# Optimization experiments

Measured on AMD Instinct MI355X. Metric: run time of the kernel, lower is better.

## Reference

```python
import jax, jax.numpy as jnp
import numpy as np

N, E, T, F, H, OUT, HORIZON = 50000, 1600000, 12, 16, 128, 3, 6
TARGET_IDX = (0, 1, 2)


def setup_inputs() -> dict:
    key = jax.random.key(0)
    ks = jax.random.split(key, 20)
    inp = {
        'x_seq': jax.random.normal(ks[0], (T, N, F), jnp.float32),
        'ei_seq': jax.random.randint(ks[1], (T, 2, E), 0, N, jnp.int32),
        'ea_seq': jax.random.uniform(ks[2], (T, E), jnp.float32),
        'mask_seq': jax.random.bernoulli(ks[3], 0.9, (T, N)),
    }
    sF = 1.0 / np.sqrt(F)
    s2H = 1.0 / np.sqrt(2 * H)
    sH = 1.0 / np.sqrt(H)
    # GCNConv weights (x @ W, W: [F,H]) + biases for z, r, h gates
    for i, g in enumerate(['z', 'r', 'h']):
        inp['Wc' + g] = jax.random.normal(ks[4 + i], (F, H), jnp.float32) * sF
        inp['bc' + g] = jnp.zeros((H,), jnp.float32)
        # Linear(2H, H) stored as [2H, H] for x @ W
        inp['Wl' + g] = jax.random.normal(ks[8 + i], (2 * H, H), jnp.float32) * s2H
        inp['bl' + g] = jnp.zeros((H,), jnp.float32)
    inp['head_W'] = jax.random.normal(ks[12], (H, OUT), jnp.float32) * sH
    inp['head_b'] = jnp.zeros((OUT,), jnp.float32)
    return inp


def _gcn(x, src, dst, ew, W, b):
    # GCNConv with self-loops and symmetric normalization
    loop = jnp.arange(N, dtype=src.dtype)
    s = jnp.concatenate([src, loop])
    d = jnp.concatenate([dst, loop])
    w = jnp.concatenate([ew, jnp.ones((N,), ew.dtype)])
    deg = jax.ops.segment_sum(w, d, num_segments=N)
    dinv = jnp.where(deg > 0, jax.lax.rsqrt(jnp.maximum(deg, 1e-12)), 0.0)
    norm = dinv[s] * w * dinv[d]                      # [E+N]
    xw = x @ W                                        # [N,H]
    return jax.ops.segment_sum(norm[:, None] * xw[s], d, num_segments=N) + b


def _tgcn_cell(x, ei, ew, h, p):
    src, dst = ei[0], ei[1]
    z = jax.nn.sigmoid(
        jnp.concatenate([_gcn(x, src, dst, ew, p['Wcz'], p['bcz']), h], axis=1) @ p['Wlz'] + p['blz'])
    r = jax.nn.sigmoid(
        jnp.concatenate([_gcn(x, src, dst, ew, p['Wcr'], p['bcr']), h], axis=1) @ p['Wlr'] + p['blr'])
    h_tilde = jnp.tanh(
        jnp.concatenate([_gcn(x, src, dst, ew, p['Wch'], p['bch']), h * r], axis=1) @ p['Wlh'] + p['blh'])
    return z * h + (1.0 - z) * h_tilde


def reference(x_seq, ei_seq, ea_seq, mask_seq,
              Wcz, bcz, Wlz, blz, Wcr, bcr, Wlr, blr, Wch, bch, Wlh, blh,
              head_W, head_b):
    p = dict(Wcz=Wcz, bcz=bcz, Wlz=Wlz, blz=blz, Wcr=Wcr, bcr=bcr,
             Wlr=Wlr, blr=blr, Wch=Wch, bch=bch, Wlh=Wlh, blh=blh)

    def step(carry, inputs):
        h_state, seen = carry
        x, ei, ew, m = inputs
        # h_dict lookup: only nodes present now AND seen before carry state
        h_prev = jnp.where((m & seen)[:, None], h_state, 0.0)
        h_new = _tgcn_cell(x, ei, ew, h_prev, p)
        h_state = jnp.where(m[:, None], h_new, h_state)   # h_dict scatter update
        return (h_state, seen | m), None

    init = (jnp.zeros((N, H), x_seq.dtype), jnp.zeros((N,), bool))
    (h_state, _), _ = jax.lax.scan(step, init, (x_seq, ei_seq, ea_seq, mask_seq))

    # final gather: nodes present at last step are all in h_dict after the loop
    h_prev = jnp.where(mask_seq[-1][:, None], h_state, 0.0)
    x_last, ei_last, ew_last = x_seq[-1], ei_seq[-1], ea_seq[-1]
    ti = jnp.array(TARGET_IDX)
    preds = []
    for _ in range(HORIZON):
        inp = x_last if not preds else x_last.at[:, ti].set(preds[-1])
        h_new = _tgcn_cell(inp, ei_last, ew_last, h_prev, p)
        preds.append(h_new @ head_W + head_b)   # dropout is identity in eval
        h_prev = h_new
    return jnp.stack(preds, axis=0)             # [HORIZON, N, OUT]
```

## Files before the change

kernel.cpp:

```cpp
#include <hip/hip_runtime.h>
#include <math.h>

#define NN 50000
#define TT 12
#define EE 1600000
#define FF 16
#define HH 128
#define CHK 4096
#define NCH 391
#define BKT 128
#define NBINS 391
#define CAP 6144
#define RP 50016
#define CGB 782
#define AH_STR 136
#define AX_STR 40
#define HC_STR 136
#define BKROW 160

typedef _Float16 half8_t __attribute__((ext_vector_type(8)));
typedef float floatx4 __attribute__((ext_vector_type(4)));

__device__ __forceinline__ float h16_to_f(unsigned short u) {
    _Float16 h; __builtin_memcpy(&h, &u, 2); return (float)h;
}
__device__ __forceinline__ unsigned short f_to_h16(float f) {
    _Float16 h = (_Float16)f; unsigned short u; __builtin_memcpy(&u, &h, 2); return u;
}
__device__ __forceinline__ float fsig(float x) {
    return 1.0f / (1.0f + exp2f(-1.44269504f * x));
}
__device__ __forceinline__ float ftanh(float x) {
    return 2.0f / (1.0f + exp2f(-2.88539009f * x)) - 1.0f;
}

__global__ void detect_mask(const unsigned char* __restrict__ m, int* __restrict__ flag) {
    __shared__ int cnt[2];
    if (threadIdx.x < 2) cnt[threadIdx.x] = 0;
    __syncthreads();
    int a = 0, b = 0;
    for (int base = 0; base < 4096; base += 256) {
        int idx = base + threadIdx.x;
        unsigned char v = m[idx];
        int r = idx & 3;
        if (v) { if (r == 0) a++; else if (r == 1) b++; }
    }
    atomicAdd(&cnt[0], a);
    atomicAdd(&cnt[1], b);
    __syncthreads();
    if (threadIdx.x == 0) flag[0] = cnt[1] > 0 ? 0 : (cnt[0] > 0 ? 1 : 2);
}

__global__ void build_masks(const void* __restrict__ mask, const int* __restrict__ flag,
                            unsigned char* __restrict__ hm, unsigned char* __restrict__ mc) {
    int n = blockIdx.x * 256 + threadIdx.x;
    if (n >= NN) return;
    int mode = flag[0];
    bool seen = false;
    for (int t = 0; t < TT; t++) {
        int idx = t * NN + n;
        bool m;
        if (mode == 0)      m = ((const unsigned char*)mask)[idx] != 0;
        else if (mode == 1) m = ((const int*)mask)[idx] != 0;
        else                m = ((const float*)mask)[idx] != 0.0f;
        hm[idx] = (m && seen) ? 1 : 0;
        mc[idx] = m ? 1 : 0;
        seen = seen || m;
    }
}

__global__ void hist_kernel(const int* __restrict__ ei, int* __restrict__ chunkHist) {
    __shared__ int h[NBINS + 1];
    int c = blockIdx.x, t = blockIdx.y, tid = threadIdx.x;
    for (int i = tid; i < NBINS; i += 256) h[i] = 0;
    __syncthreads();
    const int* dstp = ei + (size_t)(2 * t + 1) * EE;
    int e0 = c * CHK;
    for (int i = tid; i < CHK; i += 256) {
        int e = e0 + i;
        if (e < EE) atomicAdd(&h[dstp[e] >> 7], 1);
    }
    __syncthreads();
    for (int i = tid; i < NBINS; i += 256)
        chunkHist[((size_t)t * NBINS + i) * NCH + c] = h[i];
}

__global__ void scan_kernel(int* __restrict__ buf) {
    __shared__ int ps[1024];
    const int L = NBINS * NCH;
    const int PER = 150;
    int t = blockIdx.x, tid = threadIdx.x;
    int* a = buf + (size_t)t * L;
    int i0 = tid * PER, i1 = min(i0 + PER, L);
    int s = 0;
    for (int i = i0; i < i1; i++) s += a[i];
    ps[tid] = s;
    __syncthreads();
    for (int off = 1; off < 1024; off <<= 1) {
        int v = (tid >= off) ? ps[tid - off] : 0;
        __syncthreads();
        ps[tid] += v;
        __syncthreads();
    }
    int base = (tid == 0) ? 0 : ps[tid - 1];
    for (int i = i0; i < i1; i++) { int v = a[i]; a[i] = base; base += v; }
}

__launch_bounds__(256)
__global__ void scatter_kernel(const int* __restrict__ ei, const float* __restrict__ ea,
                               const int* __restrict__ chunkOff, uint2* __restrict__ E2,
                               int batch) {
    __shared__ uint2 sorted[CHK];
    __shared__ int cnt[NBINS];
    __shared__ int sA[NBINS], sB[NBINS];
    __shared__ int start[NBINS], gbase[NBINS];
    int c = blockIdx.x, y = blockIdx.y, tid = threadIdx.x;
    int t = batch * 6 + y;
    for (int i = tid; i < NBINS; i += 256) {
        cnt[i] = 0;
        gbase[i] = chunkOff[((size_t)t * NBINS + i) * NCH + c];
    }
    __syncthreads();
    const int* srcp = ei + (size_t)(2 * t) * EE;
    const int* dstp = ei + (size_t)(2 * t + 1) * EE;
    const float* wp = ea + (size_t)t * EE;
    int e0 = c * CHK;
    int m = min(CHK, EE - e0);
    uint2 rec[16];
    int rank[16];
#pragma unroll
    for (int k = 0; k < 16; k++) {
        int i = k * 256 + tid;
        rank[k] = -1;
        if (i < m) {
            int e = e0 + i;
            unsigned int s = (unsigned int)srcp[e];
            unsigned int d = (unsigned int)dstp[e];
            float wv = wp[e];
            rec[k].x = s | (d << 16);
            rec[k].y = __float_as_uint(wv);
            rank[k] = atomicAdd(&cnt[d >> 7], 1);
        }
    }
    __syncthreads();
    for (int i = tid; i < NBINS; i += 256) sA[i] = cnt[i];
    __syncthreads();
    int pp = 0;
    for (int off = 1; off < NBINS; off <<= 1) {
        if (pp == 0) {
            for (int i = tid; i < NBINS; i += 256)
                sB[i] = (i >= off) ? sA[i] + sA[i - off] : sA[i];
        } else {
            for (int i = tid; i < NBINS; i += 256)
                sA[i] = (i >= off) ? sB[i] + sB[i - off] : sB[i];
        }
        pp ^= 1;
        __syncthreads();
    }
    const int* inc = pp ? sB : sA;
    for (int i = tid; i < NBINS; i += 256) start[i] = inc[i] - cnt[i];
    __syncthreads();
#pragma unroll
    for (int k = 0; k < 16; k++) {
        if (rank[k] >= 0) {
            int b = rec[k].x >> 23;
            sorted[start[b] + rank[k]] = rec[k];
        }
    }
    __syncthreads();
    uint2* outp = E2 + (size_t)y * EE;
    for (int i = tid; i < m; i += 256) {
        uint2 r = sorted[i];
        int b = r.x >> 23;
        outp[gbase[b] + (i - start[b])] = r;
    }
}

__launch_bounds__(256)
__global__ void sortbin_kernel(const uint2* __restrict__ E2, const int* __restrict__ chunkHist,
                               unsigned int* __restrict__ E1, int* __restrict__ rowptr,
                               float* __restrict__ dinvG, int batch) {
    __shared__ uint2 es[CAP];
    __shared__ int cnt[BKT];
    __shared__ float wsm[BKT];
    __shared__ int cur[BKT];
    int b = blockIdx.x, y = blockIdx.y, tid = threadIdx.x;
    int t = batch * 6 + y;
    const uint2* gE = E2 + (size_t)y * EE;
    unsigned int* oE = E1 + (size_t)t * EE;
    const int* off = chunkHist + (size_t)t * NBINS * NCH;
    int e0 = off[b * NCH];
    int e1 = (b == NBINS - 1) ? EE : off[(b + 1) * NCH];
    int seg = e1 - e0;
    for (int i = tid; i < seg; i += 256) es[i] = gE[e0 + i];
    if (tid < BKT) { cnt[tid] = 0; wsm[tid] = 0.0f; }
    __syncthreads();
    for (int i = tid; i < seg; i += 256) {
        int dl = (es[i].x >> 16) & 127;
        atomicAdd(&cnt[dl], 1);
        atomicAdd(&wsm[dl], __uint_as_float(es[i].y));
    }
    __syncthreads();
    int ogv = (tid < BKT) ? cnt[tid] : 0;
    for (int o = 1; o < BKT; o <<= 1) {
        int u = (tid < BKT && tid >= o) ? cnt[tid - o] : 0;
        __syncthreads();
        if (tid < BKT) cnt[tid] += u;
        __syncthreads();
    }
    if (tid < BKT) {
        int exc = cnt[tid] - ogv;
        cur[tid] = exc;
        float dv = rsqrtf(1.0f + wsm[tid]);
        wsm[tid] = dv;
        int node = b * BKT + tid;
        if (node <= NN) {
            rowptr[(size_t)t * RP + node] = e0 + exc;
            if (node < NN) dinvG[(size_t)t * NN + node] = dv;
        }
    }
    __syncthreads();
    for (int i = tid; i < seg; i += 256) {
        uint2 p = es[i];
        int dl = (p.x >> 16) & 127;
        int pos = atomicAdd(&cur[dl], 1);
        float wv = __uint_as_float(p.y) * wsm[dl];
        oE[e0 + pos] = (p.x & 0xFFFF) | ((unsigned int)f_to_h16(wv) << 16);
    }
}

__global__ void xs_kernel(const float* __restrict__ x, const float* __restrict__ dinvG,
                          _Float16* __restrict__ xs16) {
    int gid = blockIdx.x * 256 + threadIdx.x;
    int tn = gid >> 2;
    float dd = dinvG[tn];
    float4 v = ((const float4*)x)[gid];
    _Float16 h[4] = {(_Float16)(dd * v.x), (_Float16)(dd * v.y),
                     (_Float16)(dd * v.z), (_Float16)(dd * v.w)};
    uint2 o;
    __builtin_memcpy(&o, h, 8);
    ((uint2*)xs16)[gid] = o;
}

__global__ void gather_csr(const unsigned int* __restrict__ E1, const int* __restrict__ rowptr,
                           const float* __restrict__ dinvG, const _Float16* __restrict__ xs16,
                           _Float16* __restrict__ xagg16) {
    int t = blockIdx.y;
    int n = blockIdx.x * 4 + (threadIdx.x >> 6);
    if (n >= NN) return;
    int lane = threadIdx.x & 63;
    int eo = lane >> 3, fp = lane & 7;
    const unsigned int* gE = E1 + (size_t)t * EE;
    const _Float16* xs = xs16 + (size_t)t * NN * FF;
    int r0 = rowptr[(size_t)t * RP + n], r1 = rowptr[(size_t)t * RP + n + 1];
    float a0 = 0.0f, a1 = 0.0f;
    for (int e = r0 + eo; e < r1; e += 8) {
        unsigned int rec = gE[e];
        float wv = h16_to_f((unsigned short)(rec >> 16));
        unsigned int xp = *(const unsigned int*)(xs + (size_t)(rec & 0xFFFF) * FF + 2 * fp);
        a0 += wv * h16_to_f((unsigned short)(xp & 0xFFFF));
        a1 += wv * h16_to_f((unsigned short)(xp >> 16));
    }
    a0 += __shfl_xor(a0, 8);  a1 += __shfl_xor(a1, 8);
    a0 += __shfl_xor(a0, 16); a1 += __shfl_xor(a1, 16);
    a0 += __shfl_xor(a0, 32); a1 += __shfl_xor(a1, 32);
    if (eo == 0) {
        float dd = dinvG[(size_t)t * NN + n];
        unsigned int xp = *(const unsigned int*)(xs + (size_t)n * FF + 2 * fp);
        float o0 = a0 + dd * h16_to_f((unsigned short)(xp & 0xFFFF));
        float o1 = a1 + dd * h16_to_f((unsigned short)(xp >> 16));
        unsigned int pack = (unsigned int)f_to_h16(o0) | ((unsigned int)f_to_h16(o1) << 16);
        ((unsigned int*)(xagg16 + ((size_t)t * NN + n) * FF))[fp] = pack;
    }
}

__global__ void gather3_csr(const unsigned int* __restrict__ E1, const int* __restrict__ rowptr,
                            const float* __restrict__ dinvG, const float* __restrict__ predsc,
                            _Float16* __restrict__ xaggH16) {
    int n = blockIdx.x * 4 + (threadIdx.x >> 6);
    if (n >= NN) return;
    int lane = threadIdx.x & 63;
    int eo = lane >> 2, f = lane & 3;
    const unsigned int* gE = E1 + (size_t)11 * EE;
    const float* dv = dinvG + (size_t)11 * NN;
    int r0 = rowptr[(size_t)11 * RP + n], r1 = rowptr[(size_t)11 * RP + n + 1];
    float acc = 0.0f;
    for (int e = r0 + eo; e < r1; e += 16) {
        unsigned int rec = gE[e];
        float wv = h16_to_f((unsigned short)(rec >> 16));
        if (f < 3) acc += wv * predsc[(size_t)(rec & 0xFFFF) * 4 + f];
    }
    acc += __shfl_xor(acc, 4);
    acc += __shfl_xor(acc, 8);
    acc += __shfl_xor(acc, 16);
    acc += __shfl_xor(acc, 32);
    if (lane < 3) {
        float res = acc + dv[n] * predsc[(size_t)n * 4 + f];
        xaggH16[(size_t)n * FF + f] = (_Float16)res;
    }
}

__global__ void weight_kernel(const float* Wc0, const float* bc0, const float* Wl0, const float* bl0,
                              const float* Wc1, const float* bc1, const float* Wl1, const float* bl1,
                              const float* Wc2, const float* bc2, const float* Wl2, const float* bl2,
                              _Float16* __restrict__ BcatT, float* __restrict__ beff) {
    __shared__ float WcS[FF][HH];
    int g = blockIdx.x;
    int n = threadIdx.x;
    const float* Wc = g == 0 ? Wc0 : (g == 1 ? Wc1 : Wc2);
    const float* bc = g == 0 ? bc0 : (g == 1 ? bc1 : bc2);
    const float* Wl = g == 0 ? Wl0 : (g == 1 ? Wl1 : Wl2);
    const float* bl = g == 0 ? bl0 : (g == 1 ? bl1 : bl2);
    for (int q = 0; q < FF; q++) WcS[q][n] = Wc[q * HH + n];
    __syncthreads();
    float acc[FF];
#pragma unroll
    for (int i = 0; i < FF; i++) acc[i] = 0.0f;
    float accb = 0.0f;
    for (int k = 0; k < HH; k++) {
        float wl = Wl[k * HH + n];
        accb += bc[k] * wl;
#pragma unroll
        for (int i = 0; i < FF; i++) acc[i] += WcS[i][k] * wl;
    }
    _Float16* row = BcatT + ((size_t)g * HH + n) * BKROW;
    for (int j = 0; j < HH; j++) row[j] = (_Float16)Wl[(size_t)(HH + j) * HH + n];
#pragma unroll
    for (int i = 0; i < FF; i++) row[HH + i] = (_Float16)acc[i];
#pragma unroll
    for (int i = 144; i < 160; i++) row[i] = (_Float16)0.0f;
    beff[g * HH + n] = bl[n] + accb;
}

__launch_bounds__(256, 2)
__global__ void cellseq_kernel(const _Float16* __restrict__ xaggBase,
                               _Float16* __restrict__ hio,
                               const _Float16* __restrict__ BcatT,
                               const float* __restrict__ beff,
                               const unsigned char* __restrict__ hmAll,
                               const unsigned char* __restrict__ mcAll,
                               int nt) {
    __shared__ _Float16 Ah[64 * AH_STR];
    __shared__ _Float16 Ax[64 * AX_STR];
    __shared__ _Float16 Hc[64 * HC_STR];
    const int tid = threadIdx.x;
    const int m0 = blockIdx.x * 64;
    const int lane = tid & 63;
    const int w = tid >> 6;
    const int mrow = lane & 15;
    const int quad = lane >> 4;
    const int c0 = w * 32;
    const bool rec = (hmAll != nullptr);

    half8_t bz[2][5], br[2][5];
#pragma unroll
    for (int c = 0; c < 2; c++) {
        int col = c0 + c * 16 + mrow;
#pragma unroll
        for (int ks = 0; ks < 5; ks++) {
            bz[c][ks] = *(const half8_t*)(BcatT + (size_t)col * BKROW + ks * 32 + quad * 8);
            br[c][ks] = *(const half8_t*)(BcatT + (size_t)(HH + col) * BKROW + ks * 32 + quad * 8);
        }
    }
    float bzv[2], brv[2], bhv[2];
#pragma unroll
    for (int c = 0; c < 2; c++) {
        int col = c0 + c * 16 + mrow;
        bzv[c] = beff[col];
        brv[c] = beff[HH + col];
        bhv[c] = beff[2 * HH + col];
    }

    for (int idx = tid; idx < 128; idx += 256) {
        int row = idx >> 1, q = idx & 1;
        *(uint4*)(Ax + row * AX_STR + 16 + q * 8) = make_uint4(0, 0, 0, 0);
    }
    if (rec) {
        for (int idx = tid; idx < 1024; idx += 256) {
            int row = idx >> 4, q = idx & 15;
            *(uint4*)(Hc + row * HC_STR + q * 8) = make_uint4(0, 0, 0, 0);
        }
    }
    __syncthreads();

    for (int t = 0; t < nt; t++) {
        const _Float16* xa = xaggBase + (size_t)t * NN * FF;
        const unsigned char* hm = rec ? (hmAll + (size_t)t * NN) : nullptr;
        for (int idx = tid; idx < 1024; idx += 256) {
            int row = idx >> 4, q = idx & 15;
            int g = m0 + row;
            uint4 v = make_uint4(0, 0, 0, 0);
            if (rec) {
                if (g < NN && hm[g]) v = *(const uint4*)(Hc + row * HC_STR + q * 8);
            } else {
                if (g < NN) v = *(const uint4*)(hio + (size_t)g * HH + q * 8);
            }
            *(uint4*)(Ah + row * AH_STR + q * 8) = v;
        }
        for (int idx = tid; idx < 128; idx += 256) {
            int row = idx >> 1, q = idx & 1;
            int g = m0 + row;
            uint4 v = make_uint4(0, 0, 0, 0);
            if (g < NN) v = *(const uint4*)(xa + (size_t)g * FF + q * 8);
            *(uint4*)(Ax + row * AX_STR + q * 8) = v;
        }
        __syncthreads();

        floatx4 zacc[4][2], racc[4][2];
#pragma unroll
        for (int m = 0; m < 4; m++)
#pragma unroll
            for (int c = 0; c < 2; c++)
#pragma unroll
                for (int i = 0; i < 4; i++) { zacc[m][c][i] = 0.0f; racc[m][c][i] = 0.0f; }
#pragma unroll
        for (int m = 0; m < 4; m++) {
            half8_t a[5];
#pragma unroll
            for (int ks = 0; ks < 4; ks++)
                a[ks] = *(const half8_t*)(Ah + (m * 16 + mrow) * AH_STR + ks * 32 + quad * 8);
            a[4] = *(const half8_t*)(Ax + (m * 16 + mrow) * AX_STR + quad * 8);
#pragma unroll
            for (int c = 0; c < 2; c++) {
#pragma unroll
                for (int ks = 0; ks < 5; ks++)
                    zacc[m][c] = __builtin_amdgcn_mfma_f32_16x16x32_f16(a[ks], bz[c][ks], zacc[m][c], 0, 0, 0);
#pragma unroll
                for (int ks = 0; ks < 5; ks++)
                    racc[m][c] = __builtin_amdgcn_mfma_f32_16x16x32_f16(a[ks], br[c][ks], racc[m][c], 0, 0, 0);
            }
        }
        _Float16 hprev[32];
#pragma unroll
        for (int m = 0; m < 4; m++)
#pragma unroll
            for (int c = 0; c < 2; c++)
#pragma unroll
                for (int i = 0; i < 4; i++)
                    hprev[(m * 2 + c) * 4 + i] =
                        Ah[(m * 16 + quad * 4 + i) * AH_STR + c0 + c * 16 + mrow];
        __syncthreads();

        half8_t bh[2][5];
#pragma unroll
        for (int c = 0; c < 2; c++) {
            int col = c0 + c * 16 + mrow;
#pragma unroll
            for (int ks = 0; ks < 5; ks++)
                bh[c][ks] = *(const half8_t*)(BcatT + (size_t)(2 * HH + col) * BKROW + ks * 32 + quad * 8);
        }
#pragma unroll
        for (int m = 0; m < 4; m++)
#pragma unroll
            for (int c = 0; c < 2; c++)
#pragma unroll
                for (int i = 0; i < 4; i++) {
                    int row = m * 16 + quad * 4 + i;
                    float rv = fsig(racc[m][c][i] + brv[c]);
                    Ah[row * AH_STR + c0 + c * 16 + mrow] =
                        (_Float16)((float)hprev[(m * 2 + c) * 4 + i] * rv);
                }
        __syncthreads();

        floatx4 hacc[4][2];
#pragma unroll
        for (int m = 0; m < 4; m++)
#pragma unroll
            for (int c = 0; c < 2; c++)
#pragma unroll
                for (int i = 0; i < 4; i++) hacc[m][c][i] = 0.0f;
#pragma unroll
        for (int m = 0; m < 4; m++) {
            half8_t a[5];
#pragma unroll
            for (int ks = 0; ks < 4; ks++)
                a[ks] = *(const half8_t*)(Ah + (m * 16 + mrow) * AH_STR + ks * 32 + quad * 8);
            a[4] = *(const half8_t*)(Ax + (m * 16 + mrow) * AX_STR + quad * 8);
#pragma unroll
            for (int c = 0; c < 2; c++)
#pragma unroll
                for (int ks = 0; ks < 5; ks++)
                    hacc[m][c] = __builtin_amdgcn_mfma_f32_16x16x32_f16(a[ks], bh[c][ks], hacc[m][c], 0, 0, 0);
        }
        const unsigned char* mc = rec ? (mcAll + (size_t)t * NN) : nullptr;
#pragma unroll
        for (int m = 0; m < 4; m++)
#pragma unroll
            for (int c = 0; c < 2; c++)
#pragma unroll
                for (int i = 0; i < 4; i++) {
                    int row = m * 16 + quad * 4 + i;
                    int g = m0 + row;
                    if (g < NN) {
                        int col = c0 + c * 16 + mrow;
                        float z = fsig(zacc[m][c][i] + bzv[c]);
                        float ht = ftanh(hacc[m][c][i] + bhv[c]);
                        float hp = (float)hprev[(m * 2 + c) * 4 + i];
                        float hn = z * hp + (1.0f - z) * ht;
                        if (rec) {
                            if (mc[g]) Hc[row * HC_STR + col] = (_Float16)hn;
                        } else {
                            hio[(size_t)g * HH + col] = (_Float16)hn;
                        }
                    }
                }
        __syncthreads();
    }

    if (rec) {
        const unsigned char* mcL = mcAll + (size_t)(nt - 1) * NN;
        for (int idx = tid; idx < 1024; idx += 256) {
            int row = idx >> 4, q = idx & 15;
            int g = m0 + row;
            if (g < NN) {
                uint4 v = make_uint4(0, 0, 0, 0);
                if (mcL[g]) v = *(const uint4*)(Hc + row * HC_STR + q * 8);
                *(uint4*)(hio + (size_t)g * HH + q * 8) = v;
            }
        }
    }
}

__global__ void head_kernel(const _Float16* __restrict__ hp, const float* __restrict__ headW,
                            const float* __restrict__ headb, const float* __restrict__ dinv11,
                            float* __restrict__ out, float* __restrict__ predsc) {
    int node = (blockIdx.x * 256 + threadIdx.x) >> 6;
    int lane = threadIdx.x & 63;
    if (node >= NN) return;
    const _Float16* h = hp + (size_t)node * HH;
    float h0 = (float)h[lane], h1 = (float)h[64 + lane];
    float s0 = h0 * headW[lane * 3 + 0] + h1 * headW[(64 + lane) * 3 + 0];
    float s1 = h0 * headW[lane * 3 + 1] + h1 * headW[(64 + lane) * 3 + 1];
    float s2 = h0 * headW[lane * 3 + 2] + h1 * headW[(64 + lane) * 3 + 2];
#pragma unroll
    for (int off = 32; off > 0; off >>= 1) {
        s0 += __shfl_down(s0, off);
        s1 += __shfl_down(s1, off);
        s2 += __shfl_down(s2, off);
    }
    if (lane == 0) {
        float o0 = s0 + headb[0], o1 = s1 + headb[1], o2 = s2 + headb[2];
        out[(size_t)node * 3 + 0] = o0;
        out[(size_t)node * 3 + 1] = o1;
        out[(size_t)node * 3 + 2] = o2;
        float dd = dinv11[node];
        predsc[(size_t)node * 4 + 0] = dd * o0;
        predsc[(size_t)node * 4 + 1] = dd * o1;
        predsc[(size_t)node * 4 + 2] = dd * o2;
    }
}

extern "C" void kernel_launch(void* const* d_in, const int* in_sizes, int n_in,
                              void* d_out, int out_size, void* d_ws, size_t ws_size,
                              hipStream_t stream) {
    const float* x = (const float*)d_in[0];
    const int* ei = (const int*)d_in[1];
    const float* ea = (const float*)d_in[2];
    const void* mask = d_in[3];
    const float* Wc[3] = {(const float*)d_in[4], (const float*)d_in[8], (const float*)d_in[12]};
    const float* bc[3] = {(const float*)d_in[5], (const float*)d_in[9], (const float*)d_in[13]};
    const float* Wl[3] = {(const float*)d_in[6], (const float*)d_in[10], (const float*)d_in[14]};
    const float* bl[3] = {(const float*)d_in[7], (const float*)d_in[11], (const float*)d_in[15]};
    const float* headW = (const float*)d_in[16];
    const float* headb = (const float*)d_in[17];
    float* out = (float*)d_out;

    char* w = (char*)d_ws;
    auto alloc = [&](size_t bytes) {
        char* p = w;
        w += (bytes + 255) & ~(size_t)255;
        return p;
    };
    float* dinv = (float*)alloc((size_t)TT * NN * 4);
    _Float16* xagg16 = (_Float16*)alloc((size_t)TT * NN * FF * 2);
    _Float16* xaggH16 = (_Float16*)alloc((size_t)NN * FF * 2);
    _Float16* xs16 = (_Float16*)alloc((size_t)TT * NN * FF * 2);
    int* chunkHist = (int*)alloc((size_t)TT * NBINS * NCH * 4);
    int* rowptr = (int*)alloc((size_t)TT * RP * 4);
    unsigned int* E1 = (unsigned int*)alloc((size_t)TT * EE * 4);
    uint2* E2 = (uint2*)alloc((size_t)6 * EE * 8);
    _Float16* BcatT = (_Float16*)alloc((size_t)3 * HH * BKROW * 2);
    float* beff = (float*)alloc(3 * HH * 4);
    float* predsc = (float*)alloc((size_t)NN * 4 * 4);
    unsigned char* hm = (unsigned char*)alloc((size_t)TT * NN);
    unsigned char* mc = (unsigned char*)alloc((size_t)TT * NN);
    int* flag = (int*)alloc(64);

    _Float16* hph = (_Float16*)E2;

    detect_mask<<<1, 256, 0, stream>>>((const unsigned char*)mask, flag);
    build_masks<<<(NN + 255) / 256, 256, 0, stream>>>(mask, flag, hm, mc);

    hist_kernel<<<dim3(NCH, TT), 256, 0, stream>>>(ei, chunkHist);
    scan_kernel<<<TT, 1024, 0, stream>>>(chunkHist);
    for (int b = 0; b < 2; b++) {
        scatter_kernel<<<dim3(NCH, 6), 256, 0, stream>>>(ei, ea, chunkHist, E2, b);
        sortbin_kernel<<<dim3(NBINS, 6), 256, 0, stream>>>(E2, chunkHist, E1, rowptr, dinv, b);
    }
    xs_kernel<<<TT * NN * 4 / 256, 256, 0, stream>>>(x, dinv, xs16);
    gather_csr<<<dim3((NN + 3) / 4, TT), 256, 0, stream>>>(E1, rowptr, dinv, xs16, xagg16);

    weight_kernel<<<3, 128, 0, stream>>>(Wc[0], bc[0], Wl[0], bl[0],
                                         Wc[1], bc[1], Wl[1], bl[1],
                                         Wc[2], bc[2], Wl[2], bl[2], BcatT, beff);

    cellseq_kernel<<<CGB, 256, 0, stream>>>(xagg16, hph, BcatT, beff, hm, mc, TT);

    hipMemcpyAsync(xaggH16, xagg16 + (size_t)11 * NN * FF, (size_t)NN * FF * 2,
                   hipMemcpyDeviceToDevice, stream);

    for (int k = 0; k < 6; k++) {
        const _Float16* xa = (k == 0) ? (xagg16 + (size_t)11 * NN * FF) : xaggH16;
        cellseq_kernel<<<CGB, 256, 0, stream>>>(xa, hph, BcatT, beff, nullptr, nullptr, 1);
        head_kernel<<<NN * 64 / 256, 256, 0, stream>>>(hph, headW, headb, dinv + (size_t)11 * NN,
                                                       out + (size_t)k * NN * 3, predsc);
        if (k < 5) {
            gather3_csr<<<(NN + 3) / 4, 256, 0, stream>>>(E1, rowptr, dinv, predsc, xaggH16);
        }
    }
}
```

Before: 2.045 ms.

## Restructure GRU cell kernel to 512 threads with transposed MFMA operands

Doubles the cell kernel block to 8 waves, with each wave owning 16 output columns instead of 32. Gate weights are reloaded per step instead of being held in registers. The MFMA operands are swapped so each lane holds 4 contiguous columns, which enables packed 8-byte LDS and global stores. The reset-gated state goes to a separate LDS buffer, which removes one barrier per step. The aim is to cut register pressure and raise occupancy, at the cost of extra weight loads from global memory each step and more LDS per block.

```diff
diff --git a/kernel.cpp b/kernel.cpp
--- a/kernel.cpp
+++ b/kernel.cpp
@@ -332,15 +332,16 @@
     beff[g * HH + n] = bl[n] + accb;
 }
 
-__launch_bounds__(256, 2)
+__launch_bounds__(512, 4)
 __global__ void cellseq_kernel(const _Float16* __restrict__ xaggBase,
                                _Float16* __restrict__ hio,
                                const _Float16* __restrict__ BcatT,
                                const float* __restrict__ beff,
                                const unsigned char* __restrict__ hmAll,
                                const unsigned char* __restrict__ mcAll,
-                               int nt) {
+                               int nsteps) {
     __shared__ _Float16 Ah[64 * AH_STR];
+    __shared__ _Float16 Ar[64 * AH_STR];
     __shared__ _Float16 Ax[64 * AX_STR];
     __shared__ _Float16 Hc[64 * HC_STR];
     const int tid = threadIdx.x;
@@ -349,44 +350,36 @@
     const int w = tid >> 6;
     const int mrow = lane & 15;
     const int quad = lane >> 4;
-    const int c0 = w * 32;
+    const int col0 = w * 16;
+    const int cb = col0 + quad * 4;
     const bool rec = (hmAll != nullptr);
 
-    half8_t bz[2][5], br[2][5];
-#pragma unroll
-    for (int c = 0; c < 2; c++) {
-        int col = c0 + c * 16 + mrow;
-#pragma unroll
-        for (int ks = 0; ks < 5; ks++) {
-            bz[c][ks] = *(const half8_t*)(BcatT + (size_t)col * BKROW + ks * 32 + quad * 8);
-            br[c][ks] = *(const half8_t*)(BcatT + (size_t)(HH + col) * BKROW + ks * 32 + quad * 8);
-        }
-    }
-    float bzv[2], brv[2], bhv[2];
-#pragma unroll
-    for (int c = 0; c < 2; c++) {
-        int col = c0 + c * 16 + mrow;
-        bzv[c] = beff[col];
-        brv[c] = beff[HH + col];
-        bhv[c] = beff[2 * HH + col];
-    }
-
-    for (int idx = tid; idx < 128; idx += 256) {
+    const float4 bz4 = *(const float4*)(beff + cb);
+    const float4 br4 = *(const float4*)(beff + HH + cb);
+    const float4 bh4 = *(const float4*)(beff + 2 * HH + cb);
+
+    const _Float16* Wzp = BcatT + (size_t)(col0 + mrow) * BKROW + quad * 8;
+    const _Float16* Wrp = Wzp + (size_t)HH * BKROW;
+    const _Float16* Whp = Wzp + (size_t)2 * HH * BKROW;
+
+    for (int idx = tid; idx < 128; idx += 512) {
         int row = idx >> 1, q = idx & 1;
         *(uint4*)(Ax + row * AX_STR + 16 + q * 8) = make_uint4(0, 0, 0, 0);
     }
     if (rec) {
-        for (int idx = tid; idx < 1024; idx += 256) {
+        for (int idx = tid; idx < 1024; idx += 512) {
             int row = idx >> 4, q = idx & 15;
             *(uint4*)(Hc + row * HC_STR + q * 8) = make_uint4(0, 0, 0, 0);
         }
     }
     __syncthreads();
 
-    for (int t = 0; t < nt; t++) {
+    for (int t = 0; t < nsteps; t++) {
         const _Float16* xa = xaggBase + (size_t)t * NN * FF;
         const unsigned char* hm = rec ? (hmAll + (size_t)t * NN) : nullptr;
-        for (int idx = tid; idx < 1024; idx += 256) {
+        const unsigned char* mc = rec ? (mcAll + (size_t)t * NN) : nullptr;
+
+        for (int idx = tid; idx < 1024; idx += 512) {
             int row = idx >> 4, q = idx & 15;
             int g = m0 + row;
             uint4 v = make_uint4(0, 0, 0, 0);
@@ -397,7 +390,7 @@
             }
             *(uint4*)(Ah + row * AH_STR + q * 8) = v;
         }
-        for (int idx = tid; idx < 128; idx += 256) {
+        for (int idx = tid; idx < 128; idx += 512) {
             int row = idx >> 1, q = idx & 1;
             int g = m0 + row;
             uint4 v = make_uint4(0, 0, 0, 0);
@@ -406,110 +399,88 @@
         }
         __syncthreads();
 
-        floatx4 zacc[4][2], racc[4][2];
-#pragma unroll
-        for (int m = 0; m < 4; m++)
-#pragma unroll
-            for (int c = 0; c < 2; c++)
-#pragma unroll
-                for (int i = 0; i < 4; i++) { zacc[m][c][i] = 0.0f; racc[m][c][i] = 0.0f; }
-#pragma unroll
-        for (int m = 0; m < 4; m++) {
-            half8_t a[5];
-#pragma unroll
-            for (int ks = 0; ks < 4; ks++)
-                a[ks] = *(const half8_t*)(Ah + (m * 16 + mrow) * AH_STR + ks * 32 + quad * 8);
-            a[4] = *(const half8_t*)(Ax + (m * 16 + mrow) * AX_STR + quad * 8);
-#pragma unroll
-            for (int c = 0; c < 2; c++) {
-#pragma unroll
-                for (int ks = 0; ks < 5; ks++)
-                    zacc[m][c] = __builtin_amdgcn_mfma_f32_16x16x32_f16(a[ks], bz[c][ks], zacc[m][c], 0, 0, 0);
-#pragma unroll
-                for (int ks = 0; ks < 5; ks++)
-                    racc[m][c] = __builtin_amdgcn_mfma_f32_16x16x32_f16(a[ks], br[c][ks], racc[m][c], 0, 0, 0);
+        half8_t wz[5], wr[5];
+#pragma unroll
+        for (int ks = 0; ks < 5; ks++) {
+            wz[ks] = *(const half8_t*)(Wzp + ks * 32);
+            wr[ks] = *(const half8_t*)(Wrp + ks * 32);
+        }
+        floatx4 zacc[4];
+        unsigned int hpw[4][2];
+#pragma unroll
+        for (int nt = 0; nt < 4; nt++) {
+            const _Float16* hxp = Ah + (nt * 16 + mrow) * AH_STR + quad * 8;
+            half8_t hx[5];
+#pragma unroll
+            for (int ks = 0; ks < 4; ks++) hx[ks] = *(const half8_t*)(hxp + ks * 32);
+            hx[4] = *(const half8_t*)(Ax + (nt * 16 + mrow) * AX_STR + quad * 8);
+            floatx4 za = {0.0f, 0.0f, 0.0f, 0.0f}, ra = {0.0f, 0.0f, 0.0f, 0.0f};
+#pragma unroll
+            for (int ks = 0; ks < 5; ks++)
+                za = __builtin_amdgcn_mfma_f32_16x16x32_f16(wz[ks], hx[ks], za, 0, 0, 0);
+#pragma unroll
+            for (int ks = 0; ks < 5; ks++)
+                ra = __builtin_amdgcn_mfma_f32_16x16x32_f16(wr[ks], hx[ks], ra, 0, 0, 0);
+            zacc[nt] = za;
+            uint2 hp = *(const uint2*)(Ah + (nt * 16 + mrow) * AH_STR + cb);
+            hpw[nt][0] = hp.x; hpw[nt][1] = hp.y;
+            float r0 = fsig(ra[0] + br4.x), r1 = fsig(ra[1] + br4.y);
+            float r2 = fsig(ra[2] + br4.z), r3 = fsig(ra[3] + br4.w);
+            float hp0 = h16_to_f((unsigned short)(hp.x & 0xFFFF));
+            float hp1 = h16_to_f((unsigned short)(hp.x >> 16));
+            float hp2 = h16_to_f((unsigned short)(hp.y & 0xFFFF));
+            float hp3 = h16_to_f((unsigned short)(hp.y >> 16));
+            uint2 o;
+            o.x = (unsigned int)f_to_h16(hp0 * r0) | ((unsigned int)f_to_h16(hp1 * r1) << 16);
+            o.y = (unsigned int)f_to_h16(hp2 * r2) | ((unsigned int)f_to_h16(hp3 * r3) << 16);
+            *(uint2*)(Ar + (nt * 16 + mrow) * AH_STR + cb) = o;
+        }
+        __syncthreads();
+
+        half8_t wh[5];
+#pragma unroll
+        for (int ks = 0; ks < 5; ks++) wh[ks] = *(const half8_t*)(Whp + ks * 32);
+#pragma unroll
+        for (int nt = 0; nt < 4; nt++) {
+            const _Float16* hxp = Ar + (nt * 16 + mrow) * AH_STR + quad * 8;
+            half8_t hx[5];
+#pragma unroll
+            for (int ks = 0; ks < 4; ks++) hx[ks] = *(const half8_t*)(hxp + ks * 32);
+            hx[4] = *(const half8_t*)(Ax + (nt * 16 + mrow) * AX_STR + quad * 8);
+            floatx4 ha = {0.0f, 0.0f, 0.0f, 0.0f};
+#pragma unroll
+            for (int ks = 0; ks < 5; ks++)
+                ha = __builtin_amdgcn_mfma_f32_16x16x32_f16(wh[ks], hx[ks], ha, 0, 0, 0);
+            int g = m0 + nt * 16 + mrow;
+            if (g < NN) {
+                float z0 = fsig(zacc[nt][0] + bz4.x), z1 = fsig(zacc[nt][1] + bz4.y);
+                float z2 = fsig(zacc[nt][2] + bz4.z), z3 = fsig(zacc[nt][3] + bz4.w);
+                float t0 = ftanh(ha[0] + bh4.x), t1 = ftanh(ha[1] + bh4.y);
+                float t2 = ftanh(ha[2] + bh4.z), t3 = ftanh(ha[3] + bh4.w);
+                float hp0 = h16_to_f((unsigned short)(hpw[nt][0] & 0xFFFF));
+                float hp1 = h16_to_f((unsigned short)(hpw[nt][0] >> 16));
+                float hp2 = h16_to_f((unsigned short)(hpw[nt][1] & 0xFFFF));
+                float hp3 = h16_to_f((unsigned short)(hpw[nt][1] >> 16));
+                float n0 = z0 * hp0 + (1.0f - z0) * t0;
+                float n1 = z1 * hp1 + (1.0f - z1) * t1;
+                float n2 = z2 * hp2 + (1.0f - z2) * t2;
+                float n3 = z3 * hp3 + (1.0f - z3) * t3;
+                uint2 o;
+                o.x = (unsigned int)f_to_h16(n0) | ((unsigned int)f_to_h16(n1) << 16);
+                o.y = (unsigned int)f_to_h16(n2) | ((unsigned int)f_to_h16(n3) << 16);
+                if (rec) {
+                    if (mc[g]) *(uint2*)(Hc + (nt * 16 + mrow) * HC_STR + cb) = o;
+                } else {
+                    *(uint2*)(hio + (size_t)g * HH + cb) = o;
+                }
             }
         }
-        _Float16 hprev[32];
-#pragma unroll
-        for (int m = 0; m < 4; m++)
-#pragma unroll
-            for (int c = 0; c < 2; c++)
-#pragma unroll
-                for (int i = 0; i < 4; i++)
-                    hprev[(m * 2 + c) * 4 + i] =
-                        Ah[(m * 16 + quad * 4 + i) * AH_STR + c0 + c * 16 + mrow];
-        __syncthreads();
-
-        half8_t bh[2][5];
-#pragma unroll
-        for (int c = 0; c < 2; c++) {
-            int col = c0 + c * 16 + mrow;
-#pragma unroll
-            for (int ks = 0; ks < 5; ks++)
-                bh[c][ks] = *(const half8_t*)(BcatT + (size_t)(2 * HH + col) * BKROW + ks * 32 + quad * 8);
-        }
-#pragma unroll
-        for (int m = 0; m < 4; m++)
-#pragma unroll
-            for (int c = 0; c < 2; c++)
-#pragma unroll
-                for (int i = 0; i < 4; i++) {
-                    int row = m * 16 + quad * 4 + i;
-                    float rv = fsig(racc[m][c][i] + brv[c]);
-                    Ah[row * AH_STR + c0 + c * 16 + mrow] =
-                        (_Float16)((float)hprev[(m * 2 + c) * 4 + i] * rv);
-                }
-        __syncthreads();
-
-        floatx4 hacc[4][2];
-#pragma unroll
-        for (int m = 0; m < 4; m++)
-#pragma unroll
-            for (int c = 0; c < 2; c++)
-#pragma unroll
-                for (int i = 0; i < 4; i++) hacc[m][c][i] = 0.0f;
-#pragma unroll
-        for (int m = 0; m < 4; m++) {
-            half8_t a[5];
-#pragma unroll
-            for (int ks = 0; ks < 4; ks++)
-                a[ks] = *(const half8_t*)(Ah + (m * 16 + mrow) * AH_STR + ks * 32 + quad * 8);
-            a[4] = *(const half8_t*)(Ax + (m * 16 + mrow) * AX_STR + quad * 8);
-#pragma unroll
-            for (int c = 0; c < 2; c++)
-#pragma unroll
-                for (int ks = 0; ks < 5; ks++)
-                    hacc[m][c] = __builtin_amdgcn_mfma_f32_16x16x32_f16(a[ks], bh[c][ks], hacc[m][c], 0, 0, 0);
-        }
-        const unsigned char* mc = rec ? (mcAll + (size_t)t * NN) : nullptr;
-#pragma unroll
-        for (int m = 0; m < 4; m++)
-#pragma unroll
-            for (int c = 0; c < 2; c++)
-#pragma unroll
-                for (int i = 0; i < 4; i++) {
-                    int row = m * 16 + quad * 4 + i;
-                    int g = m0 + row;
-                    if (g < NN) {
-                        int col = c0 + c * 16 + mrow;
-                        float z = fsig(zacc[m][c][i] + bzv[c]);
-                        float ht = ftanh(hacc[m][c][i] + bhv[c]);
-                        float hp = (float)hprev[(m * 2 + c) * 4 + i];
-                        float hn = z * hp + (1.0f - z) * ht;
-                        if (rec) {
-                            if (mc[g]) Hc[row * HC_STR + col] = (_Float16)hn;
-                        } else {
-                            hio[(size_t)g * HH + col] = (_Float16)hn;
-                        }
-                    }
-                }
         __syncthreads();
     }
 
     if (rec) {
-        const unsigned char* mcL = mcAll + (size_t)(nt - 1) * NN;
-        for (int idx = tid; idx < 1024; idx += 256) {
+        const unsigned char* mcL = mcAll + (size_t)(nsteps - 1) * NN;
+        for (int idx = tid; idx < 1024; idx += 512) {
             int row = idx >> 4, q = idx & 15;
             int g = m0 + row;
             if (g < NN) {
@@ -604,14 +575,14 @@
                                          Wc[1], bc[1], Wl[1], bl[1],
                                          Wc[2], bc[2], Wl[2], bl[2], BcatT, beff);
 
-    cellseq_kernel<<<CGB, 256, 0, stream>>>(xagg16, hph, BcatT, beff, hm, mc, TT);
+    cellseq_kernel<<<CGB, 512, 0, stream>>>(xagg16, hph, BcatT, beff, hm, mc, TT);
 
     hipMemcpyAsync(xaggH16, xagg16 + (size_t)11 * NN * FF, (size_t)NN * FF * 2,
                    hipMemcpyDeviceToDevice, stream);
 
     for (int k = 0; k < 6; k++) {
         const _Float16* xa = (k == 0) ? (xagg16 + (size_t)11 * NN * FF) : xaggH16;
-        cellseq_kernel<<<CGB, 256, 0, stream>>>(xa, hph, BcatT, beff, nullptr, nullptr, 1);
+        cellseq_kernel<<<CGB, 512, 0, stream>>>(xa, hph, BcatT, beff, nullptr, nullptr, 1);
         head_kernel<<<NN * 64 / 256, 256, 0, stream>>>(hph, headW, headb, dinv + (size_t)11 * NN,
                                                        out + (size_t)k * NN * 3, predsc);
         if (k < 5) {
```

Measured after the change: 2.145 ms. 4.9% more time.
